# Performance work log

Measured on AMD Instinct MI355X. Metric: run time of the kernel, lower is better.

Reference implementation:

```python
import jax, jax.numpy as jnp
import numpy as np

B, S, E, H = 4, 1024, 1024, 16
D = E // H  # head_dim


def setup_inputs() -> dict:
    key = jax.random.key(0)
    ks = jax.random.split(key, 12)
    s = 1.0 / np.sqrt(E)
    return {
        "value": jax.random.normal(ks[0], (B, S, E), jnp.float32),
        "key_in": jax.random.normal(ks[1], (B, S, E), jnp.float32),
        "query": jax.random.normal(ks[2], (B, S, E), jnp.float32),
        "mask": jax.random.randint(ks[3], (B, 1, 1, S), 0, 2, jnp.int32),
        "Wq": jax.random.normal(ks[4], (E, E), jnp.float32) * s,
        "bq": jnp.zeros((E,), jnp.float32),
        "Wk": jax.random.normal(ks[5], (E, E), jnp.float32) * s,
        "bk": jnp.zeros((E,), jnp.float32),
        "Wv": jax.random.normal(ks[6], (E, E), jnp.float32) * s,
        "bv": jnp.zeros((E,), jnp.float32),
        "Wo": jax.random.normal(ks[7], (E, E), jnp.float32) * s,
        "bo": jnp.zeros((E,), jnp.float32),
    }


def reference(value, key_in, query, mask, Wq, bq, Wk, bk, Wv, bv, Wo, bo):
    b = query.shape[0]
    # torch Linear: y = x @ W.T + b
    Q = (query @ Wq.T + bq).reshape(b, query.shape[1], H, D)
    K = (key_in @ Wk.T + bk).reshape(b, key_in.shape[1], H, D)
    V = (value @ Wv.T + bv).reshape(b, value.shape[1], H, D)
    # scores scaled by 1/sqrt(embed_dim) (faithful to source, not head_dim)
    energy = jnp.einsum("bqhd,bkhd->bhqk", Q, K) / jnp.sqrt(jnp.float32(E))
    energy = jnp.where(mask == 0, jnp.float32(-1e20), energy)
    attention = jax.nn.softmax(energy, axis=-1)
    out = jnp.einsum("bhqk,bkhd->bqhd", attention, V).reshape(b, query.shape[1], E)
    return out @ Wo.T + bo
```

## Files before the change

kernel.cpp:

```cpp
#include <hip/hip_runtime.h>


typedef unsigned short u16;
typedef __bf16 bf16x8 __attribute__((ext_vector_type(8)));
typedef __bf16 bf16x2 __attribute__((ext_vector_type(2)));
typedef short s16x4 __attribute__((ext_vector_type(4)));
typedef float f32x4 __attribute__((ext_vector_type(4)));
typedef float f32x16 __attribute__((ext_vector_type(16)));

struct alignas(8) us4_t { u16 x, y, z, w; };

__device__ __forceinline__ u16 f2bf(float x) {
  unsigned int u = __builtin_bit_cast(unsigned int, x);
  unsigned int r = u + 0x7fffu + ((u >> 16) & 1u);
  return (u16)(r >> 16);
}

__device__ __forceinline__ unsigned int pack2bf(float a, float b) {
#if __has_builtin(__builtin_amdgcn_cvt_pk_bf16_f32)
  bf16x2 r = __builtin_amdgcn_cvt_pk_bf16_f32(a, b);
  return __builtin_bit_cast(unsigned int, r);
#else
  return (unsigned int)f2bf(a) | ((unsigned int)f2bf(b) << 16);
#endif
}

__device__ __forceinline__ f32x4 zero4() {
  f32x4 z; z[0] = 0.f; z[1] = 0.f; z[2] = 0.f; z[3] = 0.f; return z;
}

__device__ __forceinline__ void async_copy16(const void* g, void* l) {
  __builtin_amdgcn_global_load_lds(
      (__attribute__((address_space(1))) void*)(uintptr_t)g,
      (__attribute__((address_space(3))) void*)l, 16, 0, 0);
}

__global__ void fused_cast(const float* __restrict__ q, const float* __restrict__ k,
                           const float* __restrict__ v, const float* __restrict__ wq,
                           const float* __restrict__ wk, const float* __restrict__ wv,
                           const float* __restrict__ wo, const int* __restrict__ mask,
                           u16* __restrict__ qo, u16* __restrict__ ko, u16* __restrict__ vo,
                           u16* __restrict__ wqo, u16* __restrict__ wko, u16* __restrict__ wvo,
                           u16* __restrict__ woo, float* __restrict__ biasf) {
  const int blk = blockIdx.x;
  if (blk >= 16384) {
    int i = (blk - 16384) * 256 + threadIdx.x;
    biasf[i] = mask[i] ? 0.f : -1.4427e20f;
    return;
  }
  const float* src; u16* dst; int off;
  if (blk < 4096)       { src = q;  dst = qo;  off = blk; }
  else if (blk < 8192)  { src = k;  dst = ko;  off = blk - 4096; }
  else if (blk < 12288) { src = v;  dst = vo;  off = blk - 8192; }
  else if (blk < 13312) { src = wq; dst = wqo; off = blk - 12288; }
  else if (blk < 14336) { src = wk; dst = wko; off = blk - 13312; }
  else if (blk < 15360) { src = wv; dst = wvo; off = blk - 14336; }
  else                  { src = wo; dst = woo; off = blk - 15360; }
  const size_t i = (size_t)off * 256 + threadIdx.x;
  float4 f = ((const float4*)src)[i];
  unsigned int lo = pack2bf(f.x, f.y), hi = pack2bf(f.z, f.w);
  unsigned long long pk = (unsigned long long)lo | ((unsigned long long)hi << 32);
  ((unsigned long long*)dst)[i] = pk;
}

template <bool OUT_BF16, int NT>
__device__ __forceinline__ void gemm_core32(const u16* __restrict__ A,
                                            const u16* __restrict__ Bw,
                                            const float* __restrict__ bias,
                                            void* __restrict__ outp, bool trans,
                                            int m0, int n0) {
  __shared__ u16 lA[128 * 64];
  __shared__ u16 lB[NT * 64 * 64];
  const int tid = threadIdx.x;
  const int lane = tid & 63, w = tid >> 6;
  const int wm = w >> 1, wn = w & 1;
  const int l32 = lane & 31, hi = lane >> 5;
  const int rg = lane >> 3, cs = lane & 7;

  f32x16 acc[2][NT];
#pragma unroll
  for (int i = 0; i < 2; ++i)
#pragma unroll
    for (int j = 0; j < NT; ++j)
#pragma unroll
      for (int e = 0; e < 16; ++e) acc[i][j][e] = 0.f;

  for (int it = 0; it < 16; ++it) {
    const int k0 = it * 64;
#pragma unroll
    for (int t = 0; t < 4; ++t) {
      const int row = w * 32 + t * 8 + rg;
      const int c = cs ^ (row & 7);
      async_copy16(A + (size_t)(m0 + row) * 1024 + k0 + c * 8, &lA[(w * 32 + t * 8) * 64]);
    }
#pragma unroll
    for (int t = 0; t < NT * 2; ++t) {
      const int row = w * (NT * 16) + t * 8 + rg;
      const int c = cs ^ (row & 7);
      async_copy16(Bw + (size_t)(n0 + row) * 1024 + k0 + c * 8,
                   &lB[(w * (NT * 16) + t * 8) * 64]);
    }
    __syncthreads();
#pragma unroll
    for (int s = 0; s < 4; ++s) {
      bf16x8 af[2], bfr[NT];
#pragma unroll
      for (int i = 0; i < 2; ++i) {
        const int row = wm * 64 + i * 32 + l32;
        af[i] = *(const bf16x8*)&lA[row * 64 + (((s * 2 + hi) ^ (row & 7)) * 8)];
      }
#pragma unroll
      for (int j = 0; j < NT; ++j) {
        const int row = wn * (NT * 32) + j * 32 + l32;
        bfr[j] = *(const bf16x8*)&lB[row * 64 + (((s * 2 + hi) ^ (row & 7)) * 8)];
      }
#pragma unroll
      for (int i = 0; i < 2; ++i)
#pragma unroll
        for (int j = 0; j < NT; ++j)
          acc[i][j] = __builtin_amdgcn_mfma_f32_32x32x16_bf16(af[i], bfr[j], acc[i][j], 0, 0, 0);
    }
    __syncthreads();
  }

#pragma unroll
  for (int j = 0; j < NT; ++j) {
    const int cg = n0 + wn * (NT * 32) + j * 32 + l32;
    const float bj = bias[cg];
#pragma unroll
    for (int i = 0; i < 2; ++i) {
      const int mbase = m0 + wm * 64 + i * 32 + 4 * hi;
#pragma unroll
      for (int g = 0; g < 4; ++g) {
        const int r0 = mbase + 8 * g;
        if (!trans) {
          if (OUT_BF16) {
            u16* o = (u16*)outp;
#pragma unroll
            for (int rr = 0; rr < 4; ++rr)
              o[(size_t)(r0 + rr) * 1024 + cg] = f2bf(acc[i][j][g * 4 + rr] + bj);
          } else {
            float* o = (float*)outp;
#pragma unroll
            for (int rr = 0; rr < 4; ++rr)
              o[(size_t)(r0 + rr) * 1024 + cg] = acc[i][j][g * 4 + rr] + bj;
          }
        } else {
          u16* o = (u16*)outp;
          const int bh = ((r0 >> 10) << 4) + (cg >> 6);
          const int g2 = (r0 & 1023) >> 2;
          const int d  = cg & 63;
          union { us4_t s; unsigned int u[2]; } pk;
          pk.u[0] = pack2bf(acc[i][j][g * 4 + 0] + bj, acc[i][j][g * 4 + 1] + bj);
          pk.u[1] = pack2bf(acc[i][j][g * 4 + 2] + bj, acc[i][j][g * 4 + 3] + bj);
          *(us4_t*)&o[(size_t)bh * 65536 + g2 * 256 + d * 4] = pk.s;
        }
      }
    }
  }
}

__global__ __launch_bounds__(256, 3) void qkv_gemm(
    const u16* __restrict__ Xq, const u16* __restrict__ Xk, const u16* __restrict__ Xv,
    const u16* __restrict__ Wq, const u16* __restrict__ Wk, const u16* __restrict__ Wv,
    const float* __restrict__ bq, const float* __restrict__ bk, const float* __restrict__ bv,
    u16* __restrict__ Qo, u16* __restrict__ Ko, u16* __restrict__ Vto) {
  const int flat = blockIdx.x;
  const int xcd = flat & 7, t = flat >> 3;
  const int n = t & 7, bandl = t >> 3;
  const int band = xcd * 12 + bandl;
  const int z = band >> 5, m = band & 31;
  const u16* A = (z == 0) ? Xq : (z == 1) ? Xk : Xv;
  const u16* W = (z == 0) ? Wq : (z == 1) ? Wk : Wv;
  const float* bias = (z == 0) ? bq : (z == 1) ? bk : bv;
  u16* out = (z == 0) ? Qo : (z == 1) ? Ko : Vto;
  gemm_core32<true, 2>(A, W, bias, out, z == 2, m * 128, n * 128);
}

__global__ __launch_bounds__(256, 2) void out_gemm(
    const u16* __restrict__ A, const u16* __restrict__ W,
    const float* __restrict__ bias, float* __restrict__ out) {
  const int flat = blockIdx.x;
  const int xcd = flat & 7, t = flat >> 3;
  const int n = t & 15, m = xcd * 4 + (t >> 4);
  gemm_core32<false, 1>(A, W, bias, out, false, m * 128, n * 64);
}

__global__ __launch_bounds__(256, 4) void attn_kernel(
    const u16* __restrict__ Qb, const u16* __restrict__ Kb, const u16* __restrict__ Vtb,
    const float* __restrict__ biasf, u16* __restrict__ Ob) {
  __shared__ u16 lK[128 * 64];
  __shared__ u16 lV[64 * 128];
  u16* lQ = lV;

  const int tid = threadIdx.x;
  const int lane = tid & 63, w = tid >> 6;
  const int quad = lane >> 4, l16 = lane & 15;
  const int rg = lane >> 3, cs = lane & 7;

  const int flat = blockIdx.x;
  const int xcd = flat & 7, r = flat >> 3;
  const int bh = xcd * 8 + (r & 7), qt = r >> 3;
  const int b = bh >> 4;
  const size_t qkBase = (size_t)b * 1048576 + (size_t)(bh & 15) * 64;
  const size_t vBase = (size_t)bh * 65536;
  const float C = 0.0450842200277982f;
  const float* bp = biasf + b * 1024 + quad * 4;

#pragma unroll
  for (int t = 0; t < 2; ++t) {
    const int row = w * 16 + t * 8 + rg;
    const int c = cs ^ (row & 7);
    async_copy16(Qb + qkBase + (size_t)(qt * 64 + row) * 1024 + c * 8,
                 &lQ[(w * 16 + t * 8) * 64]);
  }
  __syncthreads();

  bf16x8 qf[2];
#pragma unroll
  for (int kk = 0; kk < 2; ++kk) {
    const int row = w * 16 + l16;
    qf[kk] = *(const bf16x8*)&lQ[row * 64 + (((kk * 4 + quad) ^ (row & 7)) * 8)];
  }
  __syncthreads();

  float lsum = 0.f;
  f32x4 oacc[4];
#pragma unroll
  for (int dt = 0; dt < 4; ++dt) oacc[dt] = zero4();

  for (int it = 0; it < 8; ++it) {
    const int k0 = it * 128;
#pragma unroll
    for (int t = 0; t < 4; ++t) {
      const int row = w * 32 + t * 8 + rg;
      const int c = cs ^ (row & 7);
      async_copy16(Kb + qkBase + (size_t)(k0 + row) * 1024 + c * 8,
                   &lK[(w * 32 + t * 8) * 64]);
    }
#pragma unroll
    for (int t = 0; t < 4; ++t) {
      const int o16 = (w * 4 + t) * 512 + lane * 8;
      async_copy16(Vtb + vBase + (size_t)it * 8192 + o16, &lV[(w * 4 + t) * 512]);
    }
    __syncthreads();

    f32x4 sacc[8];
#pragma unroll
    for (int n = 0; n < 8; ++n) sacc[n] = zero4();
#pragma unroll
    for (int kk = 0; kk < 2; ++kk) {
#pragma unroll
      for (int n = 0; n < 8; ++n) {
        const int row = n * 16 + l16;
        bf16x8 kf = *(const bf16x8*)&lK[row * 64 + (((kk * 4 + quad) ^ (row & 7)) * 8)];
        sacc[n] = __builtin_amdgcn_mfma_f32_16x16x32_bf16(kf, qf[kk], sacc[n], 0, 0, 0);
      }
    }

    f32x4 sum4 = zero4();
#pragma unroll
    for (int n = 0; n < 8; ++n) {
      const float4 vb = *(const float4*)&bp[k0 + n * 16];
      sacc[n][0] = __builtin_amdgcn_exp2f(fmaf(sacc[n][0], C, vb.x));
      sacc[n][1] = __builtin_amdgcn_exp2f(fmaf(sacc[n][1], C, vb.y));
      sacc[n][2] = __builtin_amdgcn_exp2f(fmaf(sacc[n][2], C, vb.z));
      sacc[n][3] = __builtin_amdgcn_exp2f(fmaf(sacc[n][3], C, vb.w));
      sum4[0] += sacc[n][0]; sum4[1] += sacc[n][1];
      sum4[2] += sacc[n][2]; sum4[3] += sacc[n][3];
    }
    float rs = (sum4[0] + sum4[1]) + (sum4[2] + sum4[3]);
    rs += __shfl_xor(rs, 16);
    rs += __shfl_xor(rs, 32);
    lsum += rs;

    s16x4 pf[8];
#pragma unroll
    for (int n = 0; n < 8; ++n) {
      union { s16x4 v; unsigned int u[2]; } pu;
      pu.u[0] = pack2bf(sacc[n][0], sacc[n][1]);
      pu.u[1] = pack2bf(sacc[n][2], sacc[n][3]);
      pf[n] = pu.v;
    }

#pragma unroll
    for (int dt = 0; dt < 4; ++dt) {
      const int dbase = (dt * 16 + l16) * 4;
#pragma unroll
      for (int ks = 0; ks < 8; ++ks) {
        s16x4 vf = *(const s16x4*)&lV[(ks * 4 + quad) * 256 + dbase];
        oacc[dt] = __builtin_amdgcn_mfma_f32_16x16x16bf16_1k(vf, pf[ks], oacc[dt], 0, 0, 0);
      }
    }
    __syncthreads();
  }

  const float inv = 1.f / lsum;
  const int qg = qt * 64 + w * 16 + l16;
#pragma unroll
  for (int dt = 0; dt < 4; ++dt) {
    union { us4_t s; unsigned int u[2]; } pk;
    pk.u[0] = pack2bf(oacc[dt][0] * inv, oacc[dt][1] * inv);
    pk.u[1] = pack2bf(oacc[dt][2] * inv, oacc[dt][3] * inv);
    *(us4_t*)&Ob[qkBase + (size_t)qg * 1024 + dt * 16 + quad * 4] = pk.s;
  }
}

extern "C" void kernel_launch(void* const* d_in, const int* in_sizes, int n_in,
                              void* d_out, int out_size, void* d_ws, size_t ws_size,
                              hipStream_t stream) {
  const float* value  = (const float*)d_in[0];
  const float* key_in = (const float*)d_in[1];
  const float* query  = (const float*)d_in[2];
  const int*   mask   = (const int*)d_in[3];
  const float* Wq = (const float*)d_in[4];
  const float* bq = (const float*)d_in[5];
  const float* Wk = (const float*)d_in[6];
  const float* bk = (const float*)d_in[7];
  const float* Wv = (const float*)d_in[8];
  const float* bv = (const float*)d_in[9];
  const float* Wo = (const float*)d_in[10];
  const float* bo = (const float*)d_in[11];

  u16* ws = (u16*)d_ws;
  u16* q_bf  = ws;
  u16* k_bf  = ws + 4194304;
  u16* v_bf  = ws + 8388608;
  u16* wq_bf = ws + 12582912;
  u16* wk_bf = ws + 13631488;
  u16* wv_bf = ws + 14680064;
  u16* wo_bf = ws + 15728640;
  u16* Qbuf  = ws + 16777216;
  u16* Kbuf  = ws + 20971520;
  u16* Vtbuf = ws + 25165824;
  u16* attnb = ws + 29360128;
  float* biasf = (float*)d_out;

  fused_cast<<<16400, 256, 0, stream>>>(query, key_in, value, Wq, Wk, Wv, Wo, mask,
                                        q_bf, k_bf, v_bf, wq_bf, wk_bf, wv_bf, wo_bf,
                                        biasf);
  qkv_gemm<<<dim3(768), 256, 0, stream>>>(q_bf, k_bf, v_bf, wq_bf, wk_bf, wv_bf,
                                          bq, bk, bv, Qbuf, Kbuf, Vtbuf);
  attn_kernel<<<dim3(1024), 256, 0, stream>>>(Qbuf, Kbuf, Vtbuf, biasf, attnb);
  out_gemm<<<dim3(512), 256, 0, stream>>>(attnb, wo_bf, bo, (float*)d_out);
}
```

Before: 200.3 us.

## Replace QKV projection GEMM with 256x256-tile, 512-thread double-buffered kernel

The QKV projection now uses a new 256x256 tile kernel with 8 waves, double-buffered LDS, and async global-to-LDS copies interleaved with MFMA phases under s_setprio. It launches 192 blocks instead of 768 smaller 128x128 blocks, which raises per-tile reuse and cuts redundant global loads. The trade-off is only 192 blocks for 256 CUs, so some CUs sit idle, and 128KB of LDS per block. The out_gemm occupancy hint is also raised from 2 to 3 blocks per CU.

```diff
diff --git a/kernel.cpp b/kernel.cpp
--- a/kernel.cpp
+++ b/kernel.cpp
@@ -63,6 +63,177 @@
   ((unsigned long long*)dst)[i] = pk;
 }
 
+__global__ __launch_bounds__(512, 2) void qkv_gemm256(
+    const u16* __restrict__ Xq, const u16* __restrict__ Xk, const u16* __restrict__ Xv,
+    const u16* __restrict__ Wq, const u16* __restrict__ Wk, const u16* __restrict__ Wv,
+    const float* __restrict__ bq, const float* __restrict__ bk, const float* __restrict__ bv,
+    u16* __restrict__ Qo, u16* __restrict__ Ko, u16* __restrict__ Vto) {
+  __shared__ u16 lA[2][256 * 64];
+  __shared__ u16 lB[2][256 * 64];
+
+  const int tid = threadIdx.x;
+  const int lane = tid & 63, w = tid >> 6;
+  const int wm = w >> 2, wn = w & 3;
+  const int l16 = lane & 15, q4 = lane >> 4;
+  const int rg = lane >> 3, cs = lane & 7;
+
+  const int flat = blockIdx.x;
+  const int xcd = flat & 7, t = flat >> 3;
+  const int g = xcd * 24 + t;
+  const int mt = g >> 2, n = g & 3;
+  const int z = mt >> 4, m = mt & 15;
+  const u16* A = (z == 0) ? Xq : (z == 1) ? Xk : Xv;
+  const u16* W = (z == 0) ? Wq : (z == 1) ? Wk : Wv;
+  const float* bias = (z == 0) ? bq : (z == 1) ? bk : bv;
+  u16* out = (z == 0) ? Qo : (z == 1) ? Ko : Vto;
+  const bool trans = (z == 2);
+  const int m0 = m * 256, n0 = n * 256;
+
+  f32x4 acc[8][4];
+#pragma unroll
+  for (int i = 0; i < 8; ++i)
+#pragma unroll
+    for (int j = 0; j < 4; ++j) acc[i][j] = zero4();
+
+  auto stageA = [&](int nxt, int k0) {
+#pragma unroll
+    for (int h = 0; h < 2; ++h)
+#pragma unroll
+      for (int q = 0; q < 2; ++q) {
+        const int r0 = h * 128 + (q * 8 + w) * 8;
+        const int gr = r0 + rg;
+        const int c = cs ^ (gr & 7);
+        async_copy16(A + (size_t)(m0 + gr) * 1024 + k0 + c * 8, &lA[nxt][r0 * 64]);
+      }
+  };
+  auto stageB = [&](int nxt, int k0, int h) {
+#pragma unroll
+    for (int q = 0; q < 2; ++q) {
+      const int r0 = h * 128 + (q * 8 + w) * 8;
+      const int gr = r0 + rg;
+      const int c = cs ^ (gr & 7);
+      async_copy16(W + (size_t)(n0 + gr) * 1024 + k0 + c * 8, &lB[nxt][r0 * 64]);
+    }
+  };
+  auto rdA = [&](int cur, int mf, int ks) -> bf16x8 {
+    const int row = wm * 128 + mf * 16 + l16;
+    const int ch = ks * 4 + q4;
+    return *(const bf16x8*)&lA[cur][row * 64 + ((ch ^ (row & 7)) * 8)];
+  };
+  auto rdB = [&](int cur, int nf, int ks) -> bf16x8 {
+    const int row = wn * 64 + nf * 16 + l16;
+    const int ch = ks * 4 + q4;
+    return *(const bf16x8*)&lB[cur][row * 64 + ((ch ^ (row & 7)) * 8)];
+  };
+
+  stageA(0, 0);
+  stageB(0, 0, 0);
+  stageB(0, 0, 1);
+  __syncthreads();
+
+  bf16x8 a[4][2], b[4][2];
+  for (int kt = 0; kt < 16; ++kt) {
+    const int cur = kt & 1, nxt = cur ^ 1;
+    const bool hn = (kt < 15);
+    const int k1 = (kt + 1) * 64;
+
+#pragma unroll
+    for (int mf = 0; mf < 4; ++mf) {
+      a[mf][0] = rdA(cur, mf, 0);
+      a[mf][1] = rdA(cur, mf, 1);
+    }
+#pragma unroll
+    for (int nf = 0; nf < 2; ++nf) {
+      b[nf][0] = rdB(cur, nf, 0);
+      b[nf][1] = rdB(cur, nf, 1);
+    }
+    if (hn) stageA(nxt, k1);
+    __builtin_amdgcn_s_barrier();
+    __builtin_amdgcn_s_setprio(1);
+#pragma unroll
+    for (int mf = 0; mf < 4; ++mf)
+#pragma unroll
+      for (int nf = 0; nf < 2; ++nf)
+#pragma unroll
+        for (int ks = 0; ks < 2; ++ks)
+          acc[mf][nf] = __builtin_amdgcn_mfma_f32_16x16x32_bf16(a[mf][ks], b[nf][ks],
+                                                                acc[mf][nf], 0, 0, 0);
+    __builtin_amdgcn_s_setprio(0);
+    __builtin_amdgcn_s_barrier();
+
+#pragma unroll
+    for (int nf = 2; nf < 4; ++nf) {
+      b[nf][0] = rdB(cur, nf, 0);
+      b[nf][1] = rdB(cur, nf, 1);
+    }
+    if (hn) stageB(nxt, k1, 0);
+    __builtin_amdgcn_s_barrier();
+    __builtin_amdgcn_s_setprio(1);
+#pragma unroll
+    for (int mf = 0; mf < 4; ++mf)
+#pragma unroll
+      for (int nf = 2; nf < 4; ++nf)
+#pragma unroll
+        for (int ks = 0; ks < 2; ++ks)
+          acc[mf][nf] = __builtin_amdgcn_mfma_f32_16x16x32_bf16(a[mf][ks], b[nf][ks],
+                                                                acc[mf][nf], 0, 0, 0);
+    __builtin_amdgcn_s_setprio(0);
+    __builtin_amdgcn_s_barrier();
+
+#pragma unroll
+    for (int mf = 0; mf < 4; ++mf) {
+      a[mf][0] = rdA(cur, 4 + mf, 0);
+      a[mf][1] = rdA(cur, 4 + mf, 1);
+    }
+    if (hn) stageB(nxt, k1, 1);
+    __builtin_amdgcn_s_barrier();
+    __builtin_amdgcn_s_setprio(1);
+#pragma unroll
+    for (int mf = 0; mf < 4; ++mf)
+#pragma unroll
+      for (int nf = 0; nf < 2; ++nf)
+#pragma unroll
+        for (int ks = 0; ks < 2; ++ks)
+          acc[4 + mf][nf] = __builtin_amdgcn_mfma_f32_16x16x32_bf16(a[mf][ks], b[nf][ks],
+                                                                    acc[4 + mf][nf], 0, 0, 0);
+#pragma unroll
+    for (int mf = 0; mf < 4; ++mf)
+#pragma unroll
+      for (int nf = 2; nf < 4; ++nf)
+#pragma unroll
+        for (int ks = 0; ks < 2; ++ks)
+          acc[4 + mf][nf] = __builtin_amdgcn_mfma_f32_16x16x32_bf16(a[mf][ks], b[nf][ks],
+                                                                    acc[4 + mf][nf], 0, 0, 0);
+    __builtin_amdgcn_s_setprio(0);
+    __syncthreads();
+    __builtin_amdgcn_sched_barrier(0);
+  }
+
+  const int colbase = n0 + wn * 64;
+#pragma unroll
+  for (int nf = 0; nf < 4; ++nf) {
+    const int cg = colbase + nf * 16 + l16;
+    const float bj = bias[cg];
+#pragma unroll
+    for (int mf = 0; mf < 8; ++mf) {
+      const int r0 = m0 + wm * 128 + mf * 16 + q4 * 4;
+      if (!trans) {
+#pragma unroll
+        for (int rr = 0; rr < 4; ++rr)
+          out[(size_t)(r0 + rr) * 1024 + cg] = f2bf(acc[mf][nf][rr] + bj);
+      } else {
+        const int bh = ((r0 >> 10) << 4) + (cg >> 6);
+        const int g2 = (r0 & 1023) >> 2;
+        const int d = cg & 63;
+        union { us4_t s; unsigned int u[2]; } pk;
+        pk.u[0] = pack2bf(acc[mf][nf][0] + bj, acc[mf][nf][1] + bj);
+        pk.u[1] = pack2bf(acc[mf][nf][2] + bj, acc[mf][nf][3] + bj);
+        *(us4_t*)&out[(size_t)bh * 65536 + g2 * 256 + d * 4] = pk.s;
+      }
+    }
+  }
+}
+
 template <bool OUT_BF16, int NT>
 __device__ __forceinline__ void gemm_core32(const u16* __restrict__ A,
                                             const u16* __restrict__ Bw,
@@ -160,24 +331,7 @@
   }
 }
 
-__global__ __launch_bounds__(256, 3) void qkv_gemm(
-    const u16* __restrict__ Xq, const u16* __restrict__ Xk, const u16* __restrict__ Xv,
-    const u16* __restrict__ Wq, const u16* __restrict__ Wk, const u16* __restrict__ Wv,
-    const float* __restrict__ bq, const float* __restrict__ bk, const float* __restrict__ bv,
-    u16* __restrict__ Qo, u16* __restrict__ Ko, u16* __restrict__ Vto) {
-  const int flat = blockIdx.x;
-  const int xcd = flat & 7, t = flat >> 3;
-  const int n = t & 7, bandl = t >> 3;
-  const int band = xcd * 12 + bandl;
-  const int z = band >> 5, m = band & 31;
-  const u16* A = (z == 0) ? Xq : (z == 1) ? Xk : Xv;
-  const u16* W = (z == 0) ? Wq : (z == 1) ? Wk : Wv;
-  const float* bias = (z == 0) ? bq : (z == 1) ? bk : bv;
-  u16* out = (z == 0) ? Qo : (z == 1) ? Ko : Vto;
-  gemm_core32<true, 2>(A, W, bias, out, z == 2, m * 128, n * 128);
-}
-
-__global__ __launch_bounds__(256, 2) void out_gemm(
+__global__ __launch_bounds__(256, 3) void out_gemm(
     const u16* __restrict__ A, const u16* __restrict__ W,
     const float* __restrict__ bias, float* __restrict__ out) {
   const int flat = blockIdx.x;
@@ -339,8 +493,8 @@
   fused_cast<<<16400, 256, 0, stream>>>(query, key_in, value, Wq, Wk, Wv, Wo, mask,
                                         q_bf, k_bf, v_bf, wq_bf, wk_bf, wv_bf, wo_bf,
                                         biasf);
-  qkv_gemm<<<dim3(768), 256, 0, stream>>>(q_bf, k_bf, v_bf, wq_bf, wk_bf, wv_bf,
-                                          bq, bk, bv, Qbuf, Kbuf, Vtbuf);
+  qkv_gemm256<<<dim3(192), 512, 0, stream>>>(q_bf, k_bf, v_bf, wq_bf, wk_bf, wv_bf,
+                                             bq, bk, bv, Qbuf, Kbuf, Vtbuf);
   attn_kernel<<<dim3(1024), 256, 0, stream>>>(Qbuf, Kbuf, Vtbuf, biasf, attnb);
   out_gemm<<<dim3(512), 256, 0, stream>>>(attnb, wo_bf, bo, (float*)d_out);
 }
```

After: 205.6 us. 1.03x slower.

## Replace QKV projection GEMM with 256x256-tile, 512-thread double-buffered kernel

Applied to the files above, without the earlier changes.

Swaps the 128x128-tile QKV GEMM (768 blocks of 256 threads) for a new kernel using 256x256 output tiles, 8 waves, and a two-stage LDS double buffer. It fills LDS with async global-to-LDS copies, uses a swizzled LDS layout, and interleaves waitcnt/barrier gates with 32x32x16 bf16 MFMA bursts at raised priority. The larger tile raises arithmetic intensity and cuts global traffic, but leaves only 192 blocks, which may underfill the GPU's 256 CUs. It also raises the out_gemm occupancy hint from 2 to 3.

```diff
diff --git a/kernel.cpp b/kernel.cpp
--- a/kernel.cpp
+++ b/kernel.cpp
@@ -34,6 +34,12 @@
       (__attribute__((address_space(1))) void*)(uintptr_t)g,
       (__attribute__((address_space(3))) void*)l, 16, 0, 0);
 }
+
+#define GATE(N)                                                         \
+  do {                                                                  \
+    asm volatile("s_waitcnt vmcnt(" #N ")\n\ts_barrier" ::: "memory");  \
+    __builtin_amdgcn_sched_barrier(0);                                  \
+  } while (0)
 
 __global__ void fused_cast(const float* __restrict__ q, const float* __restrict__ k,
                            const float* __restrict__ v, const float* __restrict__ wq,
@@ -63,6 +69,169 @@
   ((unsigned long long*)dst)[i] = pk;
 }
 
+template <int MLO>
+__device__ __forceinline__ void mm8(f32x16 (&acc)[4][2], const bf16x8 (&af)[2][2],
+                                    const bf16x8 (&bfr)[2][2]) {
+  __builtin_amdgcn_s_setprio(1);
+#pragma unroll
+  for (int ks = 0; ks < 2; ++ks)
+#pragma unroll
+    for (int mf = 0; mf < 2; ++mf)
+#pragma unroll
+      for (int nf = 0; nf < 2; ++nf)
+        acc[MLO + mf][nf] = __builtin_amdgcn_mfma_f32_32x32x16_bf16(
+            af[mf][ks], bfr[nf][ks], acc[MLO + mf][nf], 0, 0, 0);
+  __builtin_amdgcn_s_setprio(0);
+}
+
+__global__ __launch_bounds__(512, 2) void qkv_gemm256(
+    const u16* __restrict__ Xq, const u16* __restrict__ Xk, const u16* __restrict__ Xv,
+    const u16* __restrict__ Wq, const u16* __restrict__ Wk, const u16* __restrict__ Wv,
+    const float* __restrict__ bq, const float* __restrict__ bk, const float* __restrict__ bv,
+    u16* __restrict__ Qo, u16* __restrict__ Ko, u16* __restrict__ Vto) {
+  __shared__ u16 lA[2][2][256 * 32];
+  __shared__ u16 lB[2][2][256 * 32];
+
+  const int tid = threadIdx.x;
+  const int lane = tid & 63, w = tid >> 6;
+  const int wm = w >> 2, wn = w & 3;
+  const int l32 = lane & 31, hi = lane >> 5;
+
+  const int flat = blockIdx.x;
+  const int xcd = flat & 7, t = flat >> 3;
+  const int g = xcd * 24 + t;
+  const int mt = g >> 2, n = g & 3;
+  const int z = mt >> 4, m = mt & 15;
+  const u16* A = (z == 0) ? Xq : (z == 1) ? Xk : Xv;
+  const u16* W = (z == 0) ? Wq : (z == 1) ? Wk : Wv;
+  const float* bias = (z == 0) ? bq : (z == 1) ? bk : bv;
+  u16* out = (z == 0) ? Qo : (z == 1) ? Ko : Vto;
+  const bool trans = (z == 2);
+  const int m0 = m * 256, n0 = n * 256;
+
+  f32x16 acc[4][2];
+#pragma unroll
+  for (int i = 0; i < 4; ++i)
+#pragma unroll
+    for (int j = 0; j < 2; ++j)
+#pragma unroll
+      for (int e = 0; e < 16; ++e) acc[i][j][e] = 0.f;
+
+  int offA[2], offB[2];
+#pragma unroll
+  for (int t2 = 0; t2 < 2; ++t2) {
+    const int row = (t2 * 8 + w) * 16 + (lane >> 2);
+    const int c2 = (lane & 3) ^ (row & 3);
+    offA[t2] = (m0 + row) * 1024 + c2 * 8;
+    offB[t2] = (n0 + row) * 1024 + c2 * 8;
+  }
+
+  const u16* cA = &lA[0][0][0];
+  const u16* cB = &lB[0][0][0];
+  u16* nA = (u16*)&lA[1][0][0];
+  u16* nB = (u16*)&lB[1][0][0];
+
+  auto stA = [&](u16* dst, int h, int k0) {
+#pragma unroll
+    for (int t2 = 0; t2 < 2; ++t2)
+      async_copy16(A + (offA[t2] + k0 + h * 32), dst + h * 8192 + (t2 * 8 + w) * 512);
+  };
+  auto stB = [&](u16* dst, int h, int k0) {
+#pragma unroll
+    for (int t2 = 0; t2 < 2; ++t2)
+      async_copy16(W + (offB[t2] + k0 + h * 32), dst + h * 8192 + (t2 * 8 + w) * 512);
+  };
+  auto rd = [&](const u16* base, int h, int row, int ks) -> bf16x8 {
+    const int pc = (ks * 2 + hi) ^ (row & 3);
+    return *(const bf16x8*)&base[h * 8192 + row * 32 + pc * 8];
+  };
+
+  stA((u16*)cA, 0, 0);
+  stB((u16*)cB, 0, 0);
+  stA((u16*)cA, 1, 0);
+  stB((u16*)cB, 1, 0);
+
+  bf16x8 af[2][2], bfr[2][2];
+  for (int kt = 0; kt < 16; ++kt) {
+    const bool st = (kt < 15);
+    const int k1 = (kt + 1) * 64;
+
+    GATE(4);
+#pragma unroll
+    for (int mf = 0; mf < 2; ++mf)
+#pragma unroll
+      for (int ks = 0; ks < 2; ++ks)
+        af[mf][ks] = rd(cA, 0, wm * 128 + mf * 32 + l32, ks);
+#pragma unroll
+    for (int nf = 0; nf < 2; ++nf)
+#pragma unroll
+      for (int ks = 0; ks < 2; ++ks)
+        bfr[nf][ks] = rd(cB, 0, wn * 64 + nf * 32 + l32, ks);
+    if (st) stA(nA, 0, k1);
+    mm8<0>(acc, af, bfr);
+
+#pragma unroll
+    for (int mf = 0; mf < 2; ++mf)
+#pragma unroll
+      for (int ks = 0; ks < 2; ++ks)
+        af[mf][ks] = rd(cA, 0, wm * 128 + (2 + mf) * 32 + l32, ks);
+    if (st) stB(nB, 0, k1);
+    mm8<2>(acc, af, bfr);
+
+    if (st) { GATE(4); } else { GATE(0); }
+#pragma unroll
+    for (int mf = 0; mf < 2; ++mf)
+#pragma unroll
+      for (int ks = 0; ks < 2; ++ks)
+        af[mf][ks] = rd(cA, 1, wm * 128 + mf * 32 + l32, ks);
+#pragma unroll
+    for (int nf = 0; nf < 2; ++nf)
+#pragma unroll
+      for (int ks = 0; ks < 2; ++ks)
+        bfr[nf][ks] = rd(cB, 1, wn * 64 + nf * 32 + l32, ks);
+    if (st) stA(nA, 1, k1);
+    mm8<0>(acc, af, bfr);
+
+#pragma unroll
+    for (int mf = 0; mf < 2; ++mf)
+#pragma unroll
+      for (int ks = 0; ks < 2; ++ks)
+        af[mf][ks] = rd(cA, 1, wm * 128 + (2 + mf) * 32 + l32, ks);
+    if (st) stB(nB, 1, k1);
+    mm8<2>(acc, af, bfr);
+
+    const u16* tA = cA; cA = nA; nA = (u16*)tA;
+    const u16* tB = cB; cB = nB; nB = (u16*)tB;
+  }
+
+#pragma unroll
+  for (int nf = 0; nf < 2; ++nf) {
+    const int cg = n0 + wn * 64 + nf * 32 + l32;
+    const float bj = bias[cg];
+#pragma unroll
+    for (int mf = 0; mf < 4; ++mf) {
+      const int mbase = m0 + wm * 128 + mf * 32 + 4 * hi;
+#pragma unroll
+      for (int g2 = 0; g2 < 4; ++g2) {
+        const int r0 = mbase + 8 * g2;
+        if (!trans) {
+#pragma unroll
+          for (int rr = 0; rr < 4; ++rr)
+            out[(size_t)(r0 + rr) * 1024 + cg] = f2bf(acc[mf][nf][g2 * 4 + rr] + bj);
+        } else {
+          const int bh = ((r0 >> 10) << 4) + (cg >> 6);
+          const int gq = (r0 & 1023) >> 2;
+          const int d = cg & 63;
+          union { us4_t s; unsigned int u[2]; } pk;
+          pk.u[0] = pack2bf(acc[mf][nf][g2 * 4 + 0] + bj, acc[mf][nf][g2 * 4 + 1] + bj);
+          pk.u[1] = pack2bf(acc[mf][nf][g2 * 4 + 2] + bj, acc[mf][nf][g2 * 4 + 3] + bj);
+          *(us4_t*)&out[(size_t)bh * 65536 + gq * 256 + d * 4] = pk.s;
+        }
+      }
+    }
+  }
+}
+
 template <bool OUT_BF16, int NT>
 __device__ __forceinline__ void gemm_core32(const u16* __restrict__ A,
                                             const u16* __restrict__ Bw,
@@ -160,24 +329,7 @@
   }
 }
 
-__global__ __launch_bounds__(256, 3) void qkv_gemm(
-    const u16* __restrict__ Xq, const u16* __restrict__ Xk, const u16* __restrict__ Xv,
-    const u16* __restrict__ Wq, const u16* __restrict__ Wk, const u16* __restrict__ Wv,
-    const float* __restrict__ bq, const float* __restrict__ bk, const float* __restrict__ bv,
-    u16* __restrict__ Qo, u16* __restrict__ Ko, u16* __restrict__ Vto) {
-  const int flat = blockIdx.x;
-  const int xcd = flat & 7, t = flat >> 3;
-  const int n = t & 7, bandl = t >> 3;
-  const int band = xcd * 12 + bandl;
-  const int z = band >> 5, m = band & 31;
-  const u16* A = (z == 0) ? Xq : (z == 1) ? Xk : Xv;
-  const u16* W = (z == 0) ? Wq : (z == 1) ? Wk : Wv;
-  const float* bias = (z == 0) ? bq : (z == 1) ? bk : bv;
-  u16* out = (z == 0) ? Qo : (z == 1) ? Ko : Vto;
-  gemm_core32<true, 2>(A, W, bias, out, z == 2, m * 128, n * 128);
-}
-
-__global__ __launch_bounds__(256, 2) void out_gemm(
+__global__ __launch_bounds__(256, 3) void out_gemm(
     const u16* __restrict__ A, const u16* __restrict__ W,
     const float* __restrict__ bias, float* __restrict__ out) {
   const int flat = blockIdx.x;
@@ -339,8 +491,8 @@
   fused_cast<<<16400, 256, 0, stream>>>(query, key_in, value, Wq, Wk, Wv, Wo, mask,
                                         q_bf, k_bf, v_bf, wq_bf, wk_bf, wv_bf, wo_bf,
                                         biasf);
-  qkv_gemm<<<dim3(768), 256, 0, stream>>>(q_bf, k_bf, v_bf, wq_bf, wk_bf, wv_bf,
-                                          bq, bk, bv, Qbuf, Kbuf, Vtbuf);
+  qkv_gemm256<<<dim3(192), 512, 0, stream>>>(q_bf, k_bf, v_bf, wq_bf, wk_bf, wv_bf,
+                                             bq, bk, bv, Qbuf, Kbuf, Vtbuf);
   attn_kernel<<<dim3(1024), 256, 0, stream>>>(Qbuf, Kbuf, Vtbuf, biasf, attnb);
   out_gemm<<<dim3(512), 256, 0, stream>>>(attnb, wo_bf, bo, (float*)d_out);
 }
```

Measured after the change: 211.4 us. +5.5%, slower.
